# Kernel tuning notes

Hardware: AMD Instinct MI355X
Metric: run time of the kernel (lower is better)

The kernel has to match this reference:

```python
import jax, jax.numpy as jnp
import numpy as np

B, T, N, F_IN, GH, LH, NC = 64, 256, 61, 3, 64, 128, 10

# NOTE: dropout layers are identity here (eval-mode semantics), as in model.eval().
# F.gelu in torch is the exact (erf) gelu -> approximate=False.

def setup_inputs() -> dict:
    key = jax.random.key(0)
    ks = jax.random.split(key, 24)
    s = lambda k, shp: jax.random.normal(k, shp, jnp.float32) * 0.05
    return {
        "x": jax.random.normal(ks[0], (B, T, N * F_IN), jnp.float32),
        "adj": jax.random.uniform(ks[1], (N, N), jnp.float32) / N,
        "W_g1": s(ks[2], (GH, F_IN)), "b_g1": s(ks[3], (GH,)),
        "W_g2": s(ks[4], (GH, GH)), "b_g2": s(ks[5], (GH,)),
        "Wih_l0": s(ks[6], (2, 4 * LH, N * GH)), "Whh_l0": s(ks[7], (2, 4 * LH, LH)),
        "bih_l0": s(ks[8], (2, 4 * LH)), "bhh_l0": s(ks[9], (2, 4 * LH)),
        "Wih_l1": s(ks[10], (2, 4 * LH, 2 * LH)), "Whh_l1": s(ks[11], (2, 4 * LH, LH)),
        "bih_l1": s(ks[12], (2, 4 * LH)), "bhh_l1": s(ks[13], (2, 4 * LH)),
        "Wa1": s(ks[14], (64, 2 * LH)), "ba1": s(ks[15], (64,)),
        "Wa2": s(ks[16], (1, 64)), "ba2": s(ks[17], (1,)),
        "Wc1": s(ks[18], (LH, 2 * LH)), "bc1": s(ks[19], (LH,)),
        "Wc2": s(ks[20], (NC, LH)), "bc2": s(ks[21], (NC,)),
    }


def _lstm_layer(inp, Wih, Whh, bih, bhh):
    # inp: [B, T, D]; Wih: [2, 4H, D]; Whh: [2, 4H, H]; gate order i,f,g,o (torch)
    outs = []
    for d in range(2):
        pre = jnp.einsum('btd,gd->btg', inp, Wih[d]) + bih[d] + bhh[d]  # [B,T,4H]
        pre_t = jnp.swapaxes(pre, 0, 1)  # [T,B,4H]
        if d == 1:
            pre_t = pre_t[::-1]
        Whh_d = Whh[d]

        def step(carry, p):
            h, c = carry
            g = p + h @ Whh_d.T
            i, f, gc, o = jnp.split(g, 4, axis=-1)
            c = jax.nn.sigmoid(f) * c + jax.nn.sigmoid(i) * jnp.tanh(gc)
            h = jax.nn.sigmoid(o) * jnp.tanh(c)
            return (h, c), h

        h0 = jnp.zeros((inp.shape[0], Whh_d.shape[-1]), inp.dtype)
        _, ys = jax.lax.scan(step, (h0, h0), pre_t)
        if d == 1:
            ys = ys[::-1]
        outs.append(jnp.swapaxes(ys, 0, 1))  # [B,T,H]
    return jnp.concatenate(outs, axis=-1)  # [B,T,2H]


def reference(x, adj, W_g1, b_g1, W_g2, b_g2,
              Wih_l0, Whh_l0, bih_l0, bhh_l0,
              Wih_l1, Whh_l1, bih_l1, bhh_l1,
              Wa1, ba1, Wa2, ba2, Wc1, bc1, Wc2, bc2):
    b, t, _ = x.shape
    h = x.reshape(b, t, N, F_IN)
    # GCN layer 1: adjacency propagate + 1x1 conv (linear over feature dim) + gelu
    h = jnp.einsum('nm,btmf->btnf', adj, h)
    h = jax.nn.gelu(h @ W_g1.T + b_g1, approximate=False)
    # GCN layer 2
    h = jnp.einsum('nm,btmf->btnf', adj, h)
    h = jax.nn.gelu(h @ W_g2.T + b_g2, approximate=False)
    seq = h.reshape(b, t, N * GH)  # [B,T,3904]
    l0 = _lstm_layer(seq, Wih_l0, Whh_l0, bih_l0, bhh_l0)
    l1 = _lstm_layer(l0, Wih_l1, Whh_l1, bih_l1, bhh_l1)  # [B,T,2H]
    # attention pooling
    scores = (jnp.tanh(l1 @ Wa1.T + ba1) @ Wa2.T + ba2).squeeze(-1)  # [B,T]
    w = jax.nn.softmax(scores, axis=1)[..., None]
    ctx = jnp.sum(l1 * w, axis=1)  # [B,2H]
    hid = jax.nn.relu(ctx @ Wc1.T + bc1)
    return hid @ Wc2.T + bc2  # [B,NC]
```

## Files before the change

### kernel.cpp

```cpp
#include <hip/hip_runtime.h>
#include <math.h>

#define B_    64
#define T_    256
#define N_    61
#define FIN_  3
#define GH_   64
#define LH_   128
#define NC_   10
#define NG_   3904
#define M_TOT 16384
#define CHUNK_M 8192
#define SUB_M   2048

typedef __attribute__((ext_vector_type(8))) short bf16x8;
typedef __attribute__((ext_vector_type(4))) float f32x4;

__device__ __forceinline__ float gelu_exact(float x) {
    return 0.5f * x * (1.0f + erff(x * 0.70710678118654752f));
}
__device__ __forceinline__ float sigmoidf_(float x) {
    return 1.0f / (1.0f + expf(-x));
}
__device__ __forceinline__ float fsig(float x) {
    return __builtin_amdgcn_rcpf(1.f + __expf(-x));
}
__device__ __forceinline__ float ftanh(float x) {
    return 2.f * __builtin_amdgcn_rcpf(1.f + __expf(-2.f * x)) - 1.f;
}
__device__ __forceinline__ unsigned short f2bf(float f) {
    unsigned int u = __float_as_uint(f);
    u = (u + 0x7FFFu + ((u >> 16) & 1u)) >> 16;
    return (unsigned short)u;
}
__device__ __forceinline__ void store_h(float* p, float v) { *p = v; }
__device__ __forceinline__ void store_h(unsigned short* p, float v) { *p = f2bf(v); }

__device__ __forceinline__ void gload_lds16(const void* g, void* l) {
    __builtin_amdgcn_global_load_lds(
        (const __attribute__((address_space(1))) unsigned int*)g,
        (__attribute__((address_space(3))) unsigned int*)l,
        16, 0, 0);
}

__device__ __forceinline__ int swz(int row, int k) { return k ^ ((row & 3) << 4); }

__device__ __forceinline__ int hswz(int row, int byteoff) { return byteoff ^ ((row & 7) << 4); }

__global__ __launch_bounds__(256) void cvt_bf16_kernel(
    const float* __restrict__ in, unsigned short* __restrict__ out, int n4)
{
    int i = blockIdx.x * 256 + threadIdx.x;
    if (i < n4) {
        float4 v = reinterpret_cast<const float4*>(in)[i];
        ushort4 o;
        o.x = f2bf(v.x); o.y = f2bf(v.y); o.z = f2bf(v.z); o.w = f2bf(v.w);
        reinterpret_cast<ushort4*>(out)[i] = o;
    }
}

__global__ __launch_bounds__(256) void cvt_adj_kernel(
    const float* __restrict__ adj, unsigned short* __restrict__ adjb)
{
    int i = blockIdx.x * 256 + threadIdx.x;
    if (i < 4096) {
        int n = i >> 6, m = i & 63;
        unsigned short v = (n < N_ && m < N_) ? f2bf(adj[n * N_ + m]) : (unsigned short)0;
        adjb[n * 64 + swz(n, m)] = v;
    }
}

__global__ __launch_bounds__(256) void cvt_w2_kernel(
    const float* __restrict__ W2, unsigned short* __restrict__ w2b)
{
    int i = blockIdx.x * 256 + threadIdx.x;
    if (i < 4096) {
        int c = i >> 6, f = i & 63;
        w2b[c * 64 + swz(c, f)] = f2bf(W2[c * 64 + f]);
    }
}

__global__ __launch_bounds__(256) void gcn_h1_kernel(
    const float* __restrict__ x, const float* __restrict__ adj,
    const float* __restrict__ W1, const float* __restrict__ b1,
    unsigned short* __restrict__ H1W, int bt_base)
{
    __shared__ float adjs[N_ * 65];
    __shared__ float h1s [N_ * 65];
    __shared__ float xs [184];
    __shared__ float axs[184];
    __shared__ float w1s[192];
    __shared__ float b1s[64];

    const int tid = threadIdx.x;
    const int bt  = bt_base + blockIdx.x;

    for (int i = tid; i < N_ * N_; i += 256) {
        int n = i / 61, m = i - n * 61;
        adjs[n * 65 + m] = adj[i];
    }
    for (int i = tid; i < N_ * FIN_; i += 256) xs[i] = x[(size_t)bt * (N_ * FIN_) + i];
    for (int i = tid; i < GH_ * FIN_; i += 256) w1s[i] = W1[i];
    if (tid < GH_) b1s[tid] = b1[tid];
    __syncthreads();

    if (tid < N_ * FIN_) {
        int n = tid / 3, f = tid - n * 3;
        float acc = 0.f;
        for (int m = 0; m < N_; ++m) acc += adjs[n * 65 + m] * xs[m * 3 + f];
        axs[tid] = acc;
    }
    __syncthreads();

    for (int u = 0; u < 16; ++u) {
        int idx = tid + u * 256;
        if (idx < N_ * GH_) {
            int m = idx >> 6, c = idx & 63;
            float acc = b1s[c];
            acc += axs[m * 3 + 0] * w1s[c * 3 + 0];
            acc += axs[m * 3 + 1] * w1s[c * 3 + 1];
            acc += axs[m * 3 + 2] * w1s[c * 3 + 2];
            h1s[m * 65 + c] = gelu_exact(acc);
        }
    }
    __syncthreads();

    unsigned short* dst = H1W + (size_t)blockIdx.x * 4096;
    for (int i = tid; i < 4096; i += 256) {
        int c = i >> 6, m = i & 63;
        unsigned short v = (m < N_) ? f2bf(h1s[m * 65 + c]) : (unsigned short)0;
        dst[c * 64 + swz(c, m)] = v;
    }
}

__global__ __launch_bounds__(256) void gcn_mix_kernel(
    const unsigned short* __restrict__ H1W,
    const unsigned short* __restrict__ adjb,
    const unsigned short* __restrict__ w2b,
    const float* __restrict__ b2,
    unsigned short* __restrict__ seqc,
    int sc_base)
{
    __shared__ unsigned short adjbs[64 * 64];
    __shared__ unsigned short b1t [128 * 64];
    __shared__ unsigned short w2bs[64 * 64];
    __shared__ unsigned short T   [128 * 64];
    __shared__ float b2s[64];

    const int tid = threadIdx.x;
    const int w   = tid >> 6;
    const int l   = tid & 63;
    const int lr  = l & 15, lk = l >> 4;
    const int p   = blockIdx.x;

    #pragma unroll
    for (int q = 0; q < 2; ++q)
        gload_lds16(adjb + q * 2048 + w * 512 + l * 8, &adjbs[q * 2048 + w * 512]);
    #pragma unroll
    for (int q = 0; q < 2; ++q)
        gload_lds16(w2b + q * 2048 + w * 512 + l * 8, &w2bs[q * 2048 + w * 512]);
    #pragma unroll
    for (int q = 0; q < 4; ++q)
        gload_lds16(H1W + (size_t)p * 8192 + q * 2048 + w * 512 + l * 8,
                    &b1t[q * 2048 + w * 512]);
    if (tid < 64) b2s[tid] = b2[tid];
    __syncthreads();

    f32x4 acc1[4][2];
    #pragma unroll
    for (int i = 0; i < 4; ++i)
        #pragma unroll
        for (int j = 0; j < 2; ++j) acc1[i][j] = (f32x4){0.f, 0.f, 0.f, 0.f};

    #pragma unroll
    for (int kk = 0; kk < 2; ++kk) {
        const int kb = kk * 32 + lk * 8;
        bf16x8 af[4], bfr[2];
        #pragma unroll
        for (int i = 0; i < 4; ++i) {
            int rn = i * 16 + lr;
            af[i] = *reinterpret_cast<const bf16x8*>(&adjbs[rn * 64 + swz(rn, kb)]);
        }
        #pragma unroll
        for (int j = 0; j < 2; ++j) {
            int rb = w * 32 + j * 16 + lr;
            bfr[j] = *reinterpret_cast<const bf16x8*>(&b1t[rb * 64 + swz(rb, kb)]);
        }
        #pragma unroll
        for (int i = 0; i < 4; ++i)
            #pragma unroll
            for (int j = 0; j < 2; ++j)
                acc1[i][j] = __builtin_amdgcn_mfma_f32_16x16x32_bf16(af[i], bfr[j], acc1[i][j], 0, 0, 0);
    }

    #pragma unroll
    for (int i = 0; i < 4; ++i) {
        #pragma unroll
        for (int j = 0; j < 2; ++j) {
            int col = w * 32 + j * 16 + lr;
            int c   = col & 63;
            int rbase = (col >> 6) * 64;
            #pragma unroll
            for (int r = 0; r < 4; ++r) {
                int n   = i * 16 + lk * 4 + r;
                int row = rbase + n;
                T[row * 64 + swz(row, c)] = f2bf(acc1[i][j][r]);
            }
        }
    }
    __syncthreads();

    f32x4 acc2[2][4];
    #pragma unroll
    for (int i = 0; i < 2; ++i)
        #pragma unroll
        for (int j = 0; j < 4; ++j) acc2[i][j] = (f32x4){0.f, 0.f, 0.f, 0.f};

    #pragma unroll
    for (int kk = 0; kk < 2; ++kk) {
        const int kb = kk * 32 + lk * 8;
        bf16x8 a2[2], bw[4];
        #pragma unroll
        for (int i = 0; i < 2; ++i) {
            int r2 = w * 32 + i * 16 + lr;
            a2[i] = *reinterpret_cast<const bf16x8*>(&T[r2 * 64 + swz(r2, kb)]);
        }
        #pragma unroll
        for (int j = 0; j < 4; ++j) {
            int co = j * 16 + lr;
            bw[j] = *reinterpret_cast<const bf16x8*>(&w2bs[co * 64 + swz(co, kb)]);
        }
        #pragma unroll
        for (int i = 0; i < 2; ++i)
            #pragma unroll
            for (int j = 0; j < 4; ++j)
                acc2[i][j] = __builtin_amdgcn_mfma_f32_16x16x32_bf16(a2[i], bw[j], acc2[i][j], 0, 0, 0);
    }

    #pragma unroll
    for (int i = 0; i < 2; ++i) {
        #pragma unroll
        for (int j = 0; j < 4; ++j) {
            int co = j * 16 + lr;
            float bias = b2s[co];
            #pragma unroll
            for (int r = 0; r < 4; ++r) {
                int row = w * 32 + i * 16 + lk * 4 + r;
                int n   = row & 63;
                if (n < N_) {
                    int btc = sc_base + p * 2 + (row >> 6);
                    seqc[(size_t)btc * NG_ + n * 64 + co] =
                        f2bf(gelu_exact(acc2[i][j][r] + bias));
                }
            }
        }
    }
}

__global__ __launch_bounds__(256) void gemm_mfma_kernel(
    const unsigned short* __restrict__ A, const unsigned short* __restrict__ W,
    const float* __restrict__ bias_a, const float* __restrict__ bias_b,
    float* __restrict__ Cout, int K, int m_base, int Mtot)
{
    __shared__ unsigned short As[128 * 32];
    __shared__ unsigned short Bs[128 * 32];

    const int tid = threadIdx.x;
    const int w   = tid >> 6;
    const int l   = tid & 63;
    const int wr  = w >> 1, wc = w & 1;
    const int lr  = l & 15, lk = l >> 4;

    const int m0 = blockIdx.x * 128;
    const int n0 = blockIdx.y * 128;

    f32x4 acc[4][4];
    #pragma unroll
    for (int i = 0; i < 4; ++i)
        #pragma unroll
        for (int j = 0; j < 4; ++j) acc[i][j] = (f32x4){0.f, 0.f, 0.f, 0.f};

    const int row_a0 = tid >> 2;
    const int cb     = (tid & 3) * 8;
    const unsigned short* aptr0 = A + (size_t)(m0 + row_a0) * K + cb;
    const unsigned short* aptr1 = A + (size_t)(m0 + row_a0 + 64) * K + cb;
    const unsigned short* bptr0 = W + (size_t)(n0 + row_a0) * K + cb;
    const unsigned short* bptr1 = W + (size_t)(n0 + row_a0 + 64) * K + cb;
    unsigned short* lA0 = &As[w * 512];
    unsigned short* lA1 = &As[2048 + w * 512];
    unsigned short* lB0 = &Bs[w * 512];
    unsigned short* lB1 = &Bs[2048 + w * 512];

    for (int k0 = 0; k0 < K; k0 += 32) {
        gload_lds16(aptr0 + k0, lA0);
        gload_lds16(aptr1 + k0, lA1);
        gload_lds16(bptr0 + k0, lB0);
        gload_lds16(bptr1 + k0, lB1);
        __syncthreads();

        bf16x8 af[4], bfr[4];
        #pragma unroll
        for (int i = 0; i < 4; ++i)
            af[i] = *reinterpret_cast<const bf16x8*>(&As[(wr * 64 + i * 16 + lr) * 32 + lk * 8]);
        #pragma unroll
        for (int j = 0; j < 4; ++j)
            bfr[j] = *reinterpret_cast<const bf16x8*>(&Bs[(wc * 64 + j * 16 + lr) * 32 + lk * 8]);
        #pragma unroll
        for (int i = 0; i < 4; ++i)
            #pragma unroll
            for (int j = 0; j < 4; ++j)
                acc[i][j] = __builtin_amdgcn_mfma_f32_16x16x32_bf16(af[i], bfr[j], acc[i][j], 0, 0, 0);
        __syncthreads();
    }

    #pragma unroll
    for (int i = 0; i < 4; ++i) {
        #pragma unroll
        for (int j = 0; j < 4; ++j) {
            int n = n0 + wc * 64 + j * 16 + lr;
            float ba = bias_a[n] + bias_b[n];
            int d = n >> 9, g = n & 511;
            #pragma unroll
            for (int r = 0; r < 4; ++r) {
                int m = m_base + m0 + wr * 64 + i * 16 + lk * 4 + r;
                Cout[((size_t)d * Mtot + m) * 512 + g] = acc[i][j][r] + ba;
            }
        }
    }
}

#define LSTM_STEP(S, PUSE)                                                          \
    {                                                                               \
        const int t_ = d ? (T_ - 1 - (S)) : (S);                                    \
        const char* hb_ = (const char*)&hbuf[cur][0];                               \
        const int rowb_ = lr * 256;                                                 \
        const int xo_   = (lr & 7) << 4;                                            \
        bf16x8 a0 = *reinterpret_cast<const bf16x8*>(hb_ + rowb_ + ((0 * 64 + lk * 16) ^ xo_)); \
        bf16x8 a1 = *reinterpret_cast<const bf16x8*>(hb_ + rowb_ + ((1 * 64 + lk * 16) ^ xo_)); \
        bf16x8 a2 = *reinterpret_cast<const bf16x8*>(hb_ + rowb_ + ((2 * 64 + lk * 16) ^ xo_)); \
        bf16x8 a3 = *reinterpret_cast<const bf16x8*>(hb_ + rowb_ + ((3 * 64 + lk * 16) ^ xo_)); \
        f32x4 acc_[4];                                                              \
        _Pragma("unroll")                                                           \
        for (int g_ = 0; g_ < 4; ++g_) acc_[g_] = PUSE[g_];                         \
        if ((S) + 2 < T_) {                                                         \
            int tn_ = d ? (T_ - 3 - (S)) : ((S) + 2);                               \
            _Pragma("unroll")                                                       \
            for (int g_ = 0; g_ < 4; ++g_)                                          \
                _Pragma("unroll")                                                   \
                for (int r_ = 0; r_ < 4; ++r_)                                      \
                    PUSE[g_][r_] = pb[((size_t)(lk * 4 + r_) * T_ + tn_) * 512 + g_ * 128]; \
        }                                                                           \
        _Pragma("unroll")                                                           \
        for (int g_ = 0; g_ < 4; ++g_) {                                            \
            acc_[g_] = __builtin_amdgcn_mfma_f32_16x16x32_bf16(a0, bw[g_][0], acc_[g_], 0, 0, 0); \
            acc_[g_] = __builtin_amdgcn_mfma_f32_16x16x32_bf16(a1, bw[g_][1], acc_[g_], 0, 0, 0); \
            acc_[g_] = __builtin_amdgcn_mfma_f32_16x16x32_bf16(a2, bw[g_][2], acc_[g_], 0, 0, 0); \
            acc_[g_] = __builtin_amdgcn_mfma_f32_16x16x32_bf16(a3, bw[g_][3], acc_[g_], 0, 0, 0); \
        }                                                                           \
        char* hn_ = (char*)&hbuf[cur ^ 1][0];                                       \
        _Pragma("unroll")                                                           \
        for (int r_ = 0; r_ < 4; ++r_) {                                            \
            float gi_ = acc_[0][r_], gf_ = acc_[1][r_];                             \
            float gv_ = acc_[2][r_], go_ = acc_[3][r_];                             \
            cst[r_] = fsig(gf_) * cst[r_] + fsig(gi_) * ftanh(gv_);                 \
            float h_ = fsig(go_) * ftanh(cst[r_]);                                  \
            int m_ = lk * 4 + r_;                                                   \
            *(unsigned short*)(hn_ + m_ * 256 + hswz(m_, unit * 2)) = f2bf(h_);     \
            store_h(&hout[((size_t)(bg * 16 + m_) * T_ + t_) * 256 + d * 128 + unit], h_); \
        }                                                                           \
        asm volatile("s_waitcnt lgkmcnt(0)" ::: "memory");                          \
        __builtin_amdgcn_s_barrier();                                               \
        __builtin_amdgcn_sched_barrier(0);                                          \
        cur ^= 1;                                                                   \
    }

template <typename OT>
__global__ __launch_bounds__(512) void lstm_kernel(
    const float* __restrict__ pre,
    const unsigned short* __restrict__ Whb,
    OT* __restrict__ hout)
{
    const int d   = blockIdx.x >> 2;
    const int bg  = blockIdx.x & 3;
    const int tid = threadIdx.x;
    const int w   = tid >> 6;
    const int l   = tid & 63;
    const int lr  = l & 15;
    const int lk  = l >> 4;
    const int unit = w * 16 + lr;

    bf16x8 bw[4][4];
    #pragma unroll
    for (int g = 0; g < 4; ++g)
        #pragma unroll
        for (int kt = 0; kt < 4; ++kt)
            bw[g][kt] = *reinterpret_cast<const bf16x8*>(
                Whb + ((size_t)d * 512 + g * 128 + unit) * 128 + kt * 32 + lk * 8);

    __shared__ unsigned short hbuf[2][16 * 128];
    for (int i = tid; i < 1024; i += 512)
        reinterpret_cast<unsigned int*>(&hbuf[0][0])[i] = 0u;

    float cst[4] = {0.f, 0.f, 0.f, 0.f};

    const float* pb = pre + ((size_t)(d * B_ + bg * 16) * T_) * 512 + unit;

    f32x4 pE[4], pO[4];
    {
        int t0 = d ? (T_ - 1) : 0;
        int t1 = d ? (T_ - 2) : 1;
        #pragma unroll
        for (int g = 0; g < 4; ++g)
            #pragma unroll
            for (int r = 0; r < 4; ++r) {
                pE[g][r] = pb[((size_t)(lk * 4 + r) * T_ + t0) * 512 + g * 128];
                pO[g][r] = pb[((size_t)(lk * 4 + r) * T_ + t1) * 512 + g * 128];
            }
    }
    __syncthreads();

    int cur = 0;
    for (int s = 0; s < T_; s += 2) {
        LSTM_STEP(s,     pE);
        LSTM_STEP(s + 1, pO);
    }
}

__global__ __launch_bounds__(256) void attn_scores_kernel(
    const float* __restrict__ l1, const float* __restrict__ Wa1,
    const float* __restrict__ ba1, const float* __restrict__ Wa2,
    const float* __restrict__ ba2, float* __restrict__ scores)
{
    const int b   = blockIdx.x;
    const int t0  = blockIdx.y * 32;
    const int tid = threadIdx.x;
    const int j   = tid & 63, kq = tid >> 6;

    float w[64];
    const float* wsrc = Wa1 + j * 256 + kq * 64;
    #pragma unroll
    for (int k = 0; k < 64; ++k) w[k] = wsrc[k];

    __shared__ __align__(16) float rows[32 * 256];
    __shared__ float part[256];

    const float4* src = reinterpret_cast<const float4*>(
        l1 + (size_t)b * T_ * 256 + (size_t)t0 * 256);
    float4* dstv = reinterpret_cast<float4*>(rows);
    #pragma unroll
    for (int q = 0; q < 8; ++q) dstv[q * 256 + tid] = src[q * 256 + tid];

    float wa2 = (tid < 64) ? Wa2[tid] : 0.f;
    float bj  = (tid < 64) ? ba1[tid] : 0.f;
    float bb2 = ba2[0];
    __syncthreads();

    for (int tl = 0; tl < 32; ++tl) {
        const float* row = &rows[tl * 256 + kq * 64];
        float acc = 0.f;
        #pragma unroll
        for (int k4 = 0; k4 < 16; ++k4) {
            float4 hv = *reinterpret_cast<const float4*>(&row[k4 * 4]);
            acc += w[k4 * 4 + 0] * hv.x + w[k4 * 4 + 1] * hv.y
                 + w[k4 * 4 + 2] * hv.z + w[k4 * 4 + 3] * hv.w;
        }
        part[tid] = acc;
        __syncthreads();
        if (tid < 64) {
            float dj = part[tid] + part[tid + 64] + part[tid + 128] + part[tid + 192];
            float sv = tanhf(dj + bj) * wa2;
            #pragma unroll
            for (int off = 32; off > 0; off >>= 1) sv += __shfl_xor(sv, off);
            if (tid == 0) scores[b * T_ + t0 + tl] = sv + bb2;
        }
        __syncthreads();
    }
}

__global__ __launch_bounds__(256) void attn_head_kernel(
    const float* __restrict__ l1, const float* __restrict__ scores,
    const float* __restrict__ Wc1, const float* __restrict__ bc1,
    const float* __restrict__ Wc2, const float* __restrict__ bc2,
    float* __restrict__ out)
{
    const int b   = blockIdx.x;
    const int tid = threadIdx.x;
    __shared__ float wsl[256];
    __shared__ float red[8];
    __shared__ float ctx[256];
    __shared__ float hid[128];
    __shared__ float wc1s[128 * 65];

    float v = scores[b * T_ + tid];
    float mx = v;
    #pragma unroll
    for (int off = 32; off > 0; off >>= 1) mx = fmaxf(mx, __shfl_xor(mx, off));
    if ((tid & 63) == 0) red[tid >> 6] = mx;
    __syncthreads();
    mx = fmaxf(fmaxf(red[0], red[1]), fmaxf(red[2], red[3]));
    float e = expf(v - mx);
    float s = e;
    #pragma unroll
    for (int off = 32; off > 0; off >>= 1) s += __shfl_xor(s, off);
    if ((tid & 63) == 0) red[4 + (tid >> 6)] = s;
    __syncthreads();
    float denom = red[4] + red[5] + red[6] + red[7];
    wsl[tid] = e / denom;
    __syncthreads();

    float acc = 0.f;
    const float* lb = l1 + (size_t)b * T_ * 256 + tid;
    #pragma unroll 4
    for (int t = 0; t < T_; ++t) acc += lb[(size_t)t * 256] * wsl[t];
    ctx[tid] = acc;
    __syncthreads();

    float hacc = (tid < 128) ? bc1[tid] : 0.f;
    for (int kb = 0; kb < 4; ++kb) {
        for (int i = tid; i < 128 * 64; i += 256) {
            int jj = i >> 6, kk = i & 63;
            wc1s[jj * 65 + kk] = Wc1[jj * 256 + kb * 64 + kk];
        }
        __syncthreads();
        if (tid < 128) {
            #pragma unroll
            for (int kk = 0; kk < 64; ++kk)
                hacc += ctx[kb * 64 + kk] * wc1s[tid * 65 + kk];
        }
        __syncthreads();
    }
    if (tid < 128) hid[tid] = fmaxf(hacc, 0.f);
    __syncthreads();

    if (tid < NC_) {
        float a = bc2[tid];
        #pragma unroll
        for (int k = 0; k < 128; ++k) a += hid[k] * Wc2[tid * 128 + k];
        out[b * NC_ + tid] = a;
    }
}

extern "C" void kernel_launch(void* const* d_in, const int* in_sizes, int n_in,
                              void* d_out, int out_size, void* d_ws, size_t ws_size,
                              hipStream_t stream)
{
    const float* x    = (const float*)d_in[0];
    const float* adj  = (const float*)d_in[1];
    const float* Wg1  = (const float*)d_in[2];
    const float* bg1  = (const float*)d_in[3];
    const float* Wg2  = (const float*)d_in[4];
    const float* bg2  = (const float*)d_in[5];
    const float* Wih0 = (const float*)d_in[6];
    const float* Whh0 = (const float*)d_in[7];
    const float* bih0 = (const float*)d_in[8];
    const float* bhh0 = (const float*)d_in[9];
    const float* Wih1 = (const float*)d_in[10];
    const float* Whh1 = (const float*)d_in[11];
    const float* bih1 = (const float*)d_in[12];
    const float* bhh1 = (const float*)d_in[13];
    const float* Wa1  = (const float*)d_in[14];
    const float* ba1  = (const float*)d_in[15];
    const float* Wa2  = (const float*)d_in[16];
    const float* ba2  = (const float*)d_in[17];
    const float* Wc1  = (const float*)d_in[18];
    const float* bc1  = (const float*)d_in[19];
    const float* Wc2  = (const float*)d_in[20];
    const float* bc2  = (const float*)d_in[21];

    char* ws = (char*)d_ws;
    unsigned short* seqb = (unsigned short*)(ws);
    unsigned short* l0b  = (unsigned short*)(ws);
    float*          l1f  = (float*)(ws + 8388608);
    float*          scr  = (float*)(ws + 25165824);
    unsigned short* H1W  = (unsigned short*)(ws + 64000000);
    unsigned short* adjb = (unsigned short*)(ws + 80777216);
    unsigned short* w2b  = (unsigned short*)(ws + 80785408);
    float*          pre  = (float*)(ws + 80793600);
    unsigned short* W0b  = (unsigned short*)(ws + 147902464);
    unsigned short* W1b  = (unsigned short*)(ws + 155897856);
    unsigned short* W0hb = (unsigned short*)(ws + 156422144);
    unsigned short* W1hb = (unsigned short*)(ws + 156684288);

    const int n0e = in_sizes[6];
    const int n1e = in_sizes[10];
    const int h0e = in_sizes[7];
    const int h1e = in_sizes[11];
    cvt_bf16_kernel<<<(n0e / 4 + 255) / 256, 256, 0, stream>>>(Wih0, W0b, n0e / 4);
    cvt_bf16_kernel<<<(n1e / 4 + 255) / 256, 256, 0, stream>>>(Wih1, W1b, n1e / 4);
    cvt_bf16_kernel<<<(h0e / 4 + 255) / 256, 256, 0, stream>>>(Whh0, W0hb, h0e / 4);
    cvt_bf16_kernel<<<(h1e / 4 + 255) / 256, 256, 0, stream>>>(Whh1, W1hb, h1e / 4);
    cvt_adj_kernel<<<16, 256, 0, stream>>>(adj, adjb);
    cvt_w2_kernel <<<16, 256, 0, stream>>>(Wg2, w2b);

    for (int ch = 0; ch < 2; ++ch) {
        int m_base = ch * CHUNK_M;
        for (int sc = 0; sc < CHUNK_M / SUB_M; ++sc) {
            gcn_h1_kernel<<<SUB_M, 256, 0, stream>>>(
                x, adj, Wg1, bg1, H1W, m_base + sc * SUB_M);
            gcn_mix_kernel<<<SUB_M / 2, 256, 0, stream>>>(
                H1W, adjb, w2b, bg2, seqb, sc * SUB_M);
        }
        gemm_mfma_kernel<<<dim3(CHUNK_M / 128, 8), 256, 0, stream>>>(
            seqb, W0b, bih0, bhh0, pre, NG_, m_base, M_TOT);
    }
    lstm_kernel<<<8, 512, 0, stream>>>(pre, W0hb, l0b);
    gemm_mfma_kernel<<<dim3(M_TOT / 128, 8), 256, 0, stream>>>(
        l0b, W1b, bih1, bhh1, pre, 256, 0, M_TOT);
    lstm_kernel<<<8, 512, 0, stream>>>(pre, W1hb, l1f);
    attn_scores_kernel<<<dim3(B_, 8), 256, 0, stream>>>(l1f, Wa1, ba1, Wa2, ba2, scr);
    attn_head_kernel<<<B_, 256, 0, stream>>>(l1f, scr, Wc1, bc1, Wc2, bc2, (float*)d_out);
}
```

Measured before the change: 1.128 ms.

## Fuse GCN layer-1 computation into the mix kernel, eliminating H1W buffer

Merges the gcn_h1 kernel into the gcn_mix kernel so each block computes the layer-1 adjacency propagation, linear and gelu for its two timesteps directly into shared memory. This removes the global H1W round trip and cuts each chunk from eight launches to one. LDS is aliased between the fp32 adjacency staging and the T buffer, so total LDS rises to about 53KB per block, which may reduce occupancy. Each block also reloads the fp32 adjacency.

```diff
diff --git a/kernel.cpp b/kernel.cpp
--- a/kernel.cpp
+++ b/kernel.cpp
@@ -11,7 +11,6 @@
 #define NG_   3904
 #define M_TOT 16384
 #define CHUNK_M 8192
-#define SUB_M   2048
 
 typedef __attribute__((ext_vector_type(8))) short bf16x8;
 typedef __attribute__((ext_vector_type(4))) float f32x4;
@@ -80,90 +79,76 @@
     }
 }
 
-__global__ __launch_bounds__(256) void gcn_h1_kernel(
+__global__ __launch_bounds__(256) void gcn_fused_kernel(
     const float* __restrict__ x, const float* __restrict__ adj,
     const float* __restrict__ W1, const float* __restrict__ b1,
-    unsigned short* __restrict__ H1W, int bt_base)
-{
-    __shared__ float adjs[N_ * 65];
-    __shared__ float h1s [N_ * 65];
-    __shared__ float xs [184];
-    __shared__ float axs[184];
-    __shared__ float w1s[192];
-    __shared__ float b1s[64];
-
-    const int tid = threadIdx.x;
-    const int bt  = bt_base + blockIdx.x;
-
-    for (int i = tid; i < N_ * N_; i += 256) {
-        int n = i / 61, m = i - n * 61;
-        adjs[n * 65 + m] = adj[i];
-    }
-    for (int i = tid; i < N_ * FIN_; i += 256) xs[i] = x[(size_t)bt * (N_ * FIN_) + i];
-    for (int i = tid; i < GH_ * FIN_; i += 256) w1s[i] = W1[i];
-    if (tid < GH_) b1s[tid] = b1[tid];
-    __syncthreads();
-
-    if (tid < N_ * FIN_) {
-        int n = tid / 3, f = tid - n * 3;
-        float acc = 0.f;
-        for (int m = 0; m < N_; ++m) acc += adjs[n * 65 + m] * xs[m * 3 + f];
-        axs[tid] = acc;
-    }
-    __syncthreads();
-
-    for (int u = 0; u < 16; ++u) {
-        int idx = tid + u * 256;
-        if (idx < N_ * GH_) {
-            int m = idx >> 6, c = idx & 63;
-            float acc = b1s[c];
-            acc += axs[m * 3 + 0] * w1s[c * 3 + 0];
-            acc += axs[m * 3 + 1] * w1s[c * 3 + 1];
-            acc += axs[m * 3 + 2] * w1s[c * 3 + 2];
-            h1s[m * 65 + c] = gelu_exact(acc);
-        }
-    }
-    __syncthreads();
-
-    unsigned short* dst = H1W + (size_t)blockIdx.x * 4096;
-    for (int i = tid; i < 4096; i += 256) {
-        int c = i >> 6, m = i & 63;
-        unsigned short v = (m < N_) ? f2bf(h1s[m * 65 + c]) : (unsigned short)0;
-        dst[c * 64 + swz(c, m)] = v;
-    }
-}
-
-__global__ __launch_bounds__(256) void gcn_mix_kernel(
-    const unsigned short* __restrict__ H1W,
     const unsigned short* __restrict__ adjb,
     const unsigned short* __restrict__ w2b,
     const float* __restrict__ b2,
     unsigned short* __restrict__ seqc,
-    int sc_base)
-{
-    __shared__ unsigned short adjbs[64 * 64];
-    __shared__ unsigned short b1t [128 * 64];
-    __shared__ unsigned short w2bs[64 * 64];
-    __shared__ unsigned short T   [128 * 64];
-    __shared__ float b2s[64];
+    int m_base)
+{
+    __shared__ __align__(16) char ldsbuf[53376];
+    float*          adjs  = (float*)(ldsbuf);
+    unsigned short* T     = (unsigned short*)(ldsbuf);
+    unsigned short* b1t   = (unsigned short*)(ldsbuf + 16384);
+    unsigned short* adjbs = (unsigned short*)(ldsbuf + 32768);
+    unsigned short* w2bs  = (unsigned short*)(ldsbuf + 40960);
+    float*          xs2   = (float*)(ldsbuf + 49152);
+    float*          axs2  = (float*)(ldsbuf + 50624);
+    float*          w1s   = (float*)(ldsbuf + 52096);
+    float*          b1s   = (float*)(ldsbuf + 52864);
+    float*          b2s   = (float*)(ldsbuf + 53120);
 
     const int tid = threadIdx.x;
     const int w   = tid >> 6;
     const int l   = tid & 63;
     const int lr  = l & 15, lk = l >> 4;
     const int p   = blockIdx.x;
+    const int bt0 = m_base + p * 2;
 
     #pragma unroll
     for (int q = 0; q < 2; ++q)
-        gload_lds16(adjb + q * 2048 + w * 512 + l * 8, &adjbs[q * 2048 + w * 512]);
+        gload_lds16(adjb + q * 2048 + w * 512 + l * 8, adjbs + q * 2048 + w * 512);
     #pragma unroll
     for (int q = 0; q < 2; ++q)
-        gload_lds16(w2b + q * 2048 + w * 512 + l * 8, &w2bs[q * 2048 + w * 512]);
-    #pragma unroll
-    for (int q = 0; q < 4; ++q)
-        gload_lds16(H1W + (size_t)p * 8192 + q * 2048 + w * 512 + l * 8,
-                    &b1t[q * 2048 + w * 512]);
-    if (tid < 64) b2s[tid] = b2[tid];
+        gload_lds16(w2b + q * 2048 + w * 512 + l * 8, w2bs + q * 2048 + w * 512);
+    for (int i = tid; i < N_ * N_; i += 256) {
+        int n = i / 61, m = i - n * 61;
+        adjs[n * 65 + m] = adj[i];
+    }
+    for (int i = tid; i < 2 * 183; i += 256) {
+        int btl = i / 183, r = i - btl * 183;
+        xs2[btl * 184 + r] = x[(size_t)(bt0 + btl) * 183 + r];
+    }
+    if (tid < 192) w1s[tid] = W1[tid];
+    if (tid < 64) { b1s[tid] = b1[tid]; b2s[tid] = b2[tid]; }
+    for (int i = tid; i < 4096; i += 256)
+        reinterpret_cast<unsigned int*>(b1t)[i] = 0u;
+    __syncthreads();
+
+    if (tid < 366) {
+        int btl = tid / 183, idx = tid - btl * 183;
+        int n = idx / 3, f = idx - n * 3;
+        float acc = 0.f;
+        for (int m = 0; m < N_; ++m) acc += adjs[n * 65 + m] * xs2[btl * 184 + m * 3 + f];
+        axs2[btl * 184 + idx] = acc;
+    }
+    __syncthreads();
+
+    for (int u = 0; u < 31; ++u) {
+        int idx = tid + u * 256;
+        if (idx < 2 * N_ * GH_) {
+            int btl = idx / NG_;
+            int r   = idx - btl * NG_;
+            int m = r >> 6, c = r & 63;
+            float acc = b1s[c];
+            acc += axs2[btl * 184 + m * 3 + 0] * w1s[c * 3 + 0];
+            acc += axs2[btl * 184 + m * 3 + 1] * w1s[c * 3 + 1];
+            acc += axs2[btl * 184 + m * 3 + 2] * w1s[c * 3 + 2];
+            b1t[(btl * 64 + c) * 64 + swz(c, m)] = f2bf(gelu_exact(acc));
+        }
+    }
     __syncthreads();
 
     f32x4 acc1[4][2];
@@ -219,7 +204,7 @@
     #pragma unroll
     for (int kk = 0; kk < 2; ++kk) {
         const int kb = kk * 32 + lk * 8;
-        bf16x8 a2[2], bw[4];
+        bf16x8 a2[2], bwv[4];
         #pragma unroll
         for (int i = 0; i < 2; ++i) {
             int r2 = w * 32 + i * 16 + lr;
@@ -228,13 +213,13 @@
         #pragma unroll
         for (int j = 0; j < 4; ++j) {
             int co = j * 16 + lr;
-            bw[j] = *reinterpret_cast<const bf16x8*>(&w2bs[co * 64 + swz(co, kb)]);
+            bwv[j] = *reinterpret_cast<const bf16x8*>(&w2bs[co * 64 + swz(co, kb)]);
         }
         #pragma unroll
         for (int i = 0; i < 2; ++i)
             #pragma unroll
             for (int j = 0; j < 4; ++j)
-                acc2[i][j] = __builtin_amdgcn_mfma_f32_16x16x32_bf16(a2[i], bw[j], acc2[i][j], 0, 0, 0);
+                acc2[i][j] = __builtin_amdgcn_mfma_f32_16x16x32_bf16(a2[i], bwv[j], acc2[i][j], 0, 0, 0);
     }
 
     #pragma unroll
@@ -248,7 +233,7 @@
                 int row = w * 32 + i * 16 + lk * 4 + r;
                 int n   = row & 63;
                 if (n < N_) {
-                    int btc = sc_base + p * 2 + (row >> 6);
+                    int btc = p * 2 + (row >> 6);
                     seqc[(size_t)btc * NG_ + n * 64 + co] =
                         f2bf(gelu_exact(acc2[i][j][r] + bias));
                 }
@@ -572,7 +557,6 @@
     unsigned short* l0b  = (unsigned short*)(ws);
     float*          l1f  = (float*)(ws + 8388608);
     float*          scr  = (float*)(ws + 25165824);
-    unsigned short* H1W  = (unsigned short*)(ws + 64000000);
     unsigned short* adjb = (unsigned short*)(ws + 80777216);
     unsigned short* w2b  = (unsigned short*)(ws + 80785408);
     float*          pre  = (float*)(ws + 80793600);
@@ -594,12 +578,8 @@
 
     for (int ch = 0; ch < 2; ++ch) {
         int m_base = ch * CHUNK_M;
-        for (int sc = 0; sc < CHUNK_M / SUB_M; ++sc) {
-            gcn_h1_kernel<<<SUB_M, 256, 0, stream>>>(
-                x, adj, Wg1, bg1, H1W, m_base + sc * SUB_M);
-            gcn_mix_kernel<<<SUB_M / 2, 256, 0, stream>>>(
-                H1W, adjb, w2b, bg2, seqb, sc * SUB_M);
-        }
+        gcn_fused_kernel<<<CHUNK_M / 2, 256, 0, stream>>>(
+            x, adj, Wg1, bg1, adjb, w2b, bg2, seqb, m_base);
         gemm_mfma_kernel<<<dim3(CHUNK_M / 128, 8), 256, 0, stream>>>(
             seqb, W0b, bih0, bhh0, pre, NG_, m_base, M_TOT);
     }
```

After: 1.018 ms (median of 2 runs). 1.11x faster.
